# Kernel tuning notes

Measured on AMD Instinct MI355X. Metric: run time of the kernel, lower is better.

The kernel has to match this reference:

```python
import jax, jax.numpy as jnp
import numpy as np

OUT = 7  # output_size (RoIPool 7x7)


def _crop_one(fm_all, roi, K):
    """Adaptive max-pool one ROI to [C, OUT, OUT].

    fm_all: [B, C, H, W]; roi: [5] int32 (batch, x1, y1, x2, y2).
    K: static max bin extent (ceil(H/OUT)+1), covers any ROI size.
    Matches torch adaptive_max_pool2d bins: start=floor(i*n/OUT), end=ceil((i+1)*n/OUT).
    """
    H, W = fm_all.shape[2], fm_all.shape[3]
    b, x1, y1, x2, y2 = roi[0], roi[1], roi[2], roi[3], roi[4]
    fm = jnp.take(fm_all, b, axis=0)  # [C, H, W]
    h = y2 - y1
    w = x2 - x1
    o = jnp.arange(OUT)
    ys = y1 + (o * h) // OUT
    ye = y1 + ((o + 1) * h + OUT - 1) // OUT  # ceil div
    xs = x1 + (o * w) // OUT
    xe = x1 + ((o + 1) * w + OUT - 1) // OUT
    k = jnp.arange(K)

    # --- pool along width (separable rectangle max) ---
    col_idx = jnp.clip(xs[:, None] + k[None, :], 0, W - 1)   # [OUT, K]
    col_valid = k[None, :] < (xe - xs)[:, None]              # [OUT, K]
    g = fm[:, :, col_idx]                                    # [C, H, OUT, K]
    g = jnp.where(col_valid, g, -jnp.inf)
    tw = g.max(axis=-1)                                      # [C, H, OUT]

    # --- pool along height ---
    row_idx = jnp.clip(ys[:, None] + k[None, :], 0, H - 1)   # [OUT, K]
    row_valid = k[None, :] < (ye - ys)[:, None]
    g2 = tw[:, row_idx, :]                                   # [C, OUT, K, OUT]
    g2 = jnp.where(row_valid[None, :, :, None], g2, -jnp.inf)
    return g2.max(axis=2)                                    # [C, OUT, OUT]


def setup_inputs() -> dict:
    key = jax.random.key(0)
    B, C, H, W, R = 2, 256, 50, 50, 192
    feature_map = jax.random.normal(key, (B, C, H, W), dtype=jnp.float32)
    rng = np.random.default_rng(0)
    batch = rng.integers(0, B, R)
    x1 = rng.integers(0, W - 1, R)
    x2 = rng.integers(x1 + 1, W + 1)  # ensure x2 > x1, <= W
    y1 = rng.integers(0, H - 1, R)
    y2 = rng.integers(y1 + 1, H + 1)
    rois = jnp.asarray(np.stack([batch, x1, y1, x2, y2], axis=1).astype(np.int32))
    return {"feature_map": feature_map, "rois": rois}


def reference(feature_map, rois):
    H = feature_map.shape[2]
    K = -(-H // OUT) + 1  # static max bin extent
    return jax.vmap(_crop_one, in_axes=(None, 0, None))(feature_map, rois, K)  # [R, C, OUT, OUT]
```

## Files before the change

kernel.cpp:

```cpp
#include <hip/hip_runtime.h>
#include <hip/hip_bf16.h>
#include <math.h>


#define OUT_N 7

__global__ __launch_bounds__(256) void roicrop_kernel(
    const float* __restrict__ fm,
    const int* __restrict__ rois,
    float* __restrict__ out,
    int R, int C, int H, int W)
{
    int idx = blockIdx.x * blockDim.x + threadIdx.x;
    int total = R * C * OUT_N * OUT_N;
    if (idx >= total) return;

    int j = idx % OUT_N;
    int t = idx / OUT_N;
    int i = t % OUT_N;
    t /= OUT_N;
    int c = t % C;
    int r = t / C;

    const int* roi = rois + r * 5;
    int b  = roi[0];
    int x1 = roi[1];
    int y1 = roi[2];
    int x2 = roi[3];
    int y2 = roi[4];
    int h = y2 - y1;
    int w = x2 - x1;

    int ys = y1 + (i * h) / OUT_N;
    int ye = y1 + ((i + 1) * h + OUT_N - 1) / OUT_N;
    int xs = x1 + (j * w) / OUT_N;
    int xe = x1 + ((j + 1) * w + OUT_N - 1) / OUT_N;

    const float* base = fm + ((size_t)(b * C + c)) * (size_t)(H * W);

    float m = -INFINITY;
    for (int y = ys; y < ye; ++y) {
        const float* rowp = base + (size_t)y * W;
        for (int x = xs; x < xe; ++x) {
            m = fmaxf(m, rowp[x]);
        }
    }
    out[idx] = m;
}

extern "C" void kernel_launch(void* const* d_in, const int* in_sizes, int n_in,
                              void* d_out, int out_size, void* d_ws, size_t ws_size,
                              hipStream_t stream)
{
    const float* fm  = (const float*)d_in[0];
    const int* rois  = (const int*)d_in[1];
    float* out       = (float*)d_out;

    const int R = in_sizes[1] / 5;
    const int C = out_size / (R * OUT_N * OUT_N);
    const int H = 50;
    const int W = 50;

    int total = R * C * OUT_N * OUT_N;
    int block = 256;
    int grid = (total + block - 1) / block;
    roicrop_kernel<<<grid, block, 0, stream>>>(fm, rois, out, R, C, H, W);
}
```

Measured before the change: 81.33 us.

## Use separable two-pass max pooling with LDS row reduction per wave

Restructures the kernel so each wave handles one channel of one ROI. In the first pass, lanes map to ROI columns and reduce vertically over each row bin with coalesced loads, writing the partial maxima to shared memory. In the second pass, threads reduce horizontally across column bins out of LDS. This removes the redundant overlapping global reads made by per-output threads. It assumes ROI width is at most 64 and C is divisible by 4, and it adds a block barrier.

New measurement: 87.48 us. +7.6%, slower.

```diff
diff --git a/kernel.cpp b/kernel.cpp
--- a/kernel.cpp
+++ b/kernel.cpp
@@ -4,6 +4,8 @@
 
 
 #define OUT_N 7
+#define CPB 4
+#define LDS_W 65
 
 __global__ __launch_bounds__(256) void roicrop_kernel(
     const float* __restrict__ fm,
@@ -11,58 +13,72 @@
     float* __restrict__ out,
     int R, int C, int H, int W)
 {
-    int idx = blockIdx.x * blockDim.x + threadIdx.x;
-    int total = R * C * OUT_N * OUT_N;
-    if (idx >= total) return;
+    __shared__ float tw[CPB][OUT_N][LDS_W];
 
-    int j = idx % OUT_N;
-    int t = idx / OUT_N;
-    int i = t % OUT_N;
-    t /= OUT_N;
-    int c = t % C;
-    int r = t / C;
+    const int lane = threadIdx.x & 63;
+    const int wave = threadIdx.x >> 6;
+    const int cg_per_r = C / CPB;
+    const int r  = blockIdx.x / cg_per_r;
+    const int cg = blockIdx.x % cg_per_r;
+    const int c  = cg * CPB + wave;
 
     const int* roi = rois + r * 5;
-    int b  = roi[0];
-    int x1 = roi[1];
-    int y1 = roi[2];
-    int x2 = roi[3];
-    int y2 = roi[4];
-    int h = y2 - y1;
-    int w = x2 - x1;
+    const int b  = roi[0];
+    const int x1 = roi[1];
+    const int y1 = roi[2];
+    const int x2 = roi[3];
+    const int y2 = roi[4];
+    const int h = y2 - y1;
+    const int w = x2 - x1;
 
-    int ys = y1 + (i * h) / OUT_N;
-    int ye = y1 + ((i + 1) * h + OUT_N - 1) / OUT_N;
-    int xs = x1 + (j * w) / OUT_N;
-    int xe = x1 + ((j + 1) * w + OUT_N - 1) / OUT_N;
+    int x = x1 + lane;
+    if (lane >= w) x = x1;
+    const float* col = fm + (size_t)(b * C + c) * (size_t)(H * W) + x;
 
-    const float* base = fm + ((size_t)(b * C + c)) * (size_t)(H * W);
+    #pragma unroll
+    for (int i = 0; i < OUT_N; ++i) {
+        const int ys = y1 + (i * h) / OUT_N;
+        const int ye = y1 + ((i + 1) * h + OUT_N - 1) / OUT_N;
+        float m = -INFINITY;
+        const float* p = col + (size_t)ys * W;
+        for (int y = ys; y < ye; ++y) {
+            m = fmaxf(m, *p);
+            p += W;
+        }
+        tw[wave][i][lane] = m;
+    }
+    __syncthreads();
 
-    float m = -INFINITY;
-    for (int y = ys; y < ye; ++y) {
-        const float* rowp = base + (size_t)y * W;
-        for (int x = xs; x < xe; ++x) {
-            m = fmaxf(m, rowp[x]);
+    const int t = threadIdx.x;
+    if (t < CPB * OUT_N * OUT_N) {
+        const int wc = t / (OUT_N * OUT_N);
+        const int l  = t % (OUT_N * OUT_N);
+        const int i  = l / OUT_N;
+        const int j  = l % OUT_N;
+        const int xs = (j * w) / OUT_N;
+        const int xe = ((j + 1) * w + OUT_N - 1) / OUT_N;
+        float m = -INFINITY;
+        for (int dx = xs; dx < xe; ++dx) {
+            m = fmaxf(m, tw[wc][i][dx]);
         }
+        const int cc = cg * CPB + wc;
+        out[((size_t)r * C + cc) * (OUT_N * OUT_N) + l] = m;
     }
-    out[idx] = m;
 }
 
 extern "C" void kernel_launch(void* const* d_in, const int* in_sizes, int n_in,
                               void* d_out, int out_size, void* d_ws, size_t ws_size,
                               hipStream_t stream)
 {
-    const float* fm  = (const float*)d_in[0];
-    const int* rois  = (const int*)d_in[1];
-    float* out       = (float*)d_out;
+    const float* fm = (const float*)d_in[0];
+    const int* rois = (const int*)d_in[1];
+    float* out      = (float*)d_out;
 
     const int R = in_sizes[1] / 5;
     const int C = out_size / (R * OUT_N * OUT_N);
     const int H = 50;
     const int W = 50;
 
-    int total = R * C * OUT_N * OUT_N;
-    int block = 256;
-    int grid = (total + block - 1) / block;
-    roicrop_kernel<<<grid, block, 0, stream>>>(fm, rois, out, R, C, H, W);
+    const int grid = R * (C / CPB);
+    roicrop_kernel<<<grid, 256, 0, stream>>>(fm, rois, out, R, C, H, W);
 }
```
